# Kernel tuning notes

Hardware: AMD Instinct MI355X
Metric: run time of the kernel (lower is better)

## Reference

```python
import jax, jax.numpy as jnp
import numpy as np

C = 512
C8 = C // 8


def setup_inputs() -> dict:
    key = jax.random.key(0)
    ks = jax.random.split(key, 7)
    B, W = 8, 2048
    x = jax.random.normal(ks[0], (B, C, W), dtype=jnp.float32)
    # 1x1 Conv1d == pointwise linear: weight [out, in], bias [out]
    s_q = 1.0 / np.sqrt(C)
    Wq = jax.random.uniform(ks[1], (C8, C), jnp.float32, -s_q, s_q)
    bq = jax.random.uniform(ks[2], (C8,), jnp.float32, -s_q, s_q)
    Wk = jax.random.uniform(ks[3], (C8, C), jnp.float32, -s_q, s_q)
    bk = jax.random.uniform(ks[4], (C8,), jnp.float32, -s_q, s_q)
    Wv = jax.random.uniform(ks[5], (C, C), jnp.float32, -s_q, s_q)
    bv = jax.random.uniform(ks[6], (C,), jnp.float32, -s_q, s_q)
    gamma = jnp.zeros((1,), dtype=jnp.float32)
    return {"x": x, "Wq": Wq, "bq": bq, "Wk": Wk, "bk": bk, "Wv": Wv, "bv": bv, "gamma": gamma}


def reference(x, Wq, bq, Wk, bk, Wv, bv, gamma):
    # x: [B, C, W]; 1x1 conv projections (pointwise linear over channel dim)
    q = jnp.einsum('oc,bcw->bwo', Wq, x) + bq            # [B, W, C/8]
    k = jnp.einsum('oc,bcw->bow', Wk, x) + bk[:, None]   # [B, C/8, W]
    v = jnp.einsum('oc,bcw->bow', Wv, x) + bv[:, None]   # [B, C, W]
    # attention[b, i, j] over keys j (no scaling, matching the original)
    attn = jax.nn.softmax(jnp.einsum('bwo,bov->bwv', q, k), axis=-1)  # [B, W, W]
    out = jnp.einsum('bcj,bij->bci', v, attn)            # [B, C, W]
    return gamma[0] * out + x
```

## Files before the change

kernel.cpp:

```cpp
#include <hip/hip_runtime.h>
#include <stdint.h>

#define B_  8
#define C_  512
#define CO_ 64
#define W_  2048
#define R_  640
#define LOG2E 1.4426950408889634f

typedef float f32x4 __attribute__((ext_vector_type(4)));
typedef float f32x16 __attribute__((ext_vector_type(16)));
typedef __bf16 bf16x8 __attribute__((ext_vector_type(8)));
typedef __bf16 bf16x2 __attribute__((ext_vector_type(2)));
typedef unsigned u32x2 __attribute__((ext_vector_type(2)));
typedef unsigned u32x4 __attribute__((ext_vector_type(4)));
typedef unsigned short u16;
typedef u16 u16x8 __attribute__((ext_vector_type(8)));
typedef u16 u16x4 __attribute__((ext_vector_type(4)));

static __device__ __forceinline__ float exp2g(float f){
  return __builtin_amdgcn_exp2f(f);
}
static __device__ __forceinline__ u16 f2b(float f){
  union { float f; unsigned u; } v; v.f = f;
  unsigned r = v.u + 0x7FFFu + ((v.u >> 16) & 1u);
  return (u16)(r >> 16);
}
static __device__ __forceinline__ bf16x8 ldb(const u16* p){
  return __builtin_bit_cast(bf16x8, *(const u16x8*)p);
}
static __device__ __forceinline__ f32x4 mfma16(bf16x8 a, bf16x8 b, f32x4 c){
  return __builtin_amdgcn_mfma_f32_16x16x32_bf16(a, b, c, 0, 0, 0);
}
static __device__ __forceinline__ f32x16 mfma32(bf16x8 a, bf16x8 b, f32x16 c){
  return __builtin_amdgcn_mfma_f32_32x32x16_bf16(a, b, c, 0, 0, 0);
}
static __device__ __forceinline__ void pl32swap(unsigned &a, unsigned &b){
  asm("v_permlane32_swap_b32 %0, %1" : "+v"(a), "+v"(b));
}
static __device__ __forceinline__ float red_sum32(float v){
  unsigned a = __builtin_bit_cast(unsigned, v), b = a;
  pl32swap(a, b);
  return __builtin_bit_cast(float, a) + __builtin_bit_cast(float, b);
}
static __device__ __forceinline__ unsigned pkbf(float lo, float hi){
  bf16x2 t; t[0] = (__bf16)lo; t[1] = (__bf16)hi;
  return __builtin_bit_cast(unsigned, t);
}
static __device__ __forceinline__ void barrier_lds_only(){
  asm volatile("s_waitcnt lgkmcnt(0)" ::: "memory");
  __builtin_amdgcn_s_barrier();
}

__global__ __launch_bounds__(256) void prep_w(
    const float* __restrict__ Wq, const float* __restrict__ bq,
    const float* __restrict__ Wk, const float* __restrict__ bk,
    const float* __restrict__ Wv, const float* __restrict__ bv,
    u16* __restrict__ Wall, float* __restrict__ ball){
  int e = blockIdx.x * 256 + threadIdx.x;
  if (e < R_ * C_){
    int r = e >> 9, c = e & (C_ - 1);
    float w;
    if (r < 64)       w = Wq[r * C_ + c] * LOG2E;
    else if (r < 128) w = Wk[(r - 64) * C_ + c];
    else              w = Wv[(r - 128) * C_ + c];
    Wall[e] = f2b(w);
  }
  if (e < R_){
    float bb;
    if (e < 64)       bb = bq[e] * LOG2E;
    else if (e < 128) bb = bk[e - 64];
    else              bb = bv[e - 128];
    ball[e] = bb;
  }
}

__global__ __launch_bounds__(256) void xpose(const float* __restrict__ x,
                                             u16* __restrict__ xbT){
  __shared__ float t[32][33];
  int b = blockIdx.z, c0 = blockIdx.y * 32, w0 = blockIdx.x * 32;
  int tx = threadIdx.x & 31, ty = threadIdx.x >> 5;
  const float* xb = x + (size_t)b * C_ * W_;
  #pragma unroll
  for (int k = 0; k < 4; k++)
    t[ty + k * 8][tx] = xb[(size_t)(c0 + ty + k * 8) * W_ + w0 + tx];
  __syncthreads();
  u16* ob = xbT + (size_t)b * W_ * C_;
  #pragma unroll
  for (int k = 0; k < 4; k++)
    ob[(size_t)(w0 + ty + k * 8) * C_ + c0 + tx] = f2b(t[tx][ty + k * 8]);
}

#define PADW 40
__global__ __launch_bounds__(256) void gemm_proj(
    const u16* __restrict__ Wall, const float* __restrict__ ball,
    const u16* __restrict__ xbT, u16* __restrict__ qf,
    u16* __restrict__ kf, u16* __restrict__ vf){
  __shared__ u16 at[64][PADW];
  __shared__ u16 bt[64][PADW];
  int b = blockIdx.z;
  int m0 = blockIdx.y * 64, n0 = blockIdx.x * 64;
  int tid = threadIdx.x, lane = tid & 63, wid = tid >> 6;
  int wm = wid >> 1, wn = wid & 1;
  int g = lane >> 4, r = lane & 15;
  const u16* xb = xbT + (size_t)b * W_ * C_;
  f32x4 acc[2][2] = {};
  int srow = tid >> 2, sseg = (tid & 3) * 8;
  for (int kk = 0; kk < 16; kk++){
    int c0 = kk * 32;
    *(u16x8*)&at[srow][sseg] = *(const u16x8*)&Wall[(size_t)(m0 + srow) * C_ + c0 + sseg];
    *(u16x8*)&bt[srow][sseg] = *(const u16x8*)&xb[(size_t)(n0 + srow) * C_ + c0 + sseg];
    barrier_lds_only();
    bf16x8 a0 = ldb(&at[wm * 32 +  0 + r][g * 8]);
    bf16x8 a1 = ldb(&at[wm * 32 + 16 + r][g * 8]);
    bf16x8 b0 = ldb(&bt[wn * 32 +  0 + r][g * 8]);
    bf16x8 b1 = ldb(&bt[wn * 32 + 16 + r][g * 8]);
    acc[0][0] = mfma16(a0, b0, acc[0][0]);
    acc[0][1] = mfma16(a0, b1, acc[0][1]);
    acc[1][0] = mfma16(a1, b0, acc[1][0]);
    acc[1][1] = mfma16(a1, b1, acc[1][1]);
    barrier_lds_only();
  }
  #pragma unroll
  for (int i = 0; i < 2; i++){
    #pragma unroll
    for (int n = 0; n < 2; n++){
      int rbase = m0 + wm * 32 + i * 16 + g * 4;
      int wcol  = n0 + wn * 32 + n * 16 + r;
      if (m0 < 128){
        u16* base = (m0 == 0 ? qf : kf) + (size_t)b * W_ * CO_;
        int o0 = (rbase & 63);
        int oc = o0 >> 4, h2 = (o0 >> 3) & 1, e0 = o0 & 7;
        u16x4 pk;
        #pragma unroll
        for (int t = 0; t < 4; t++) pk[t] = f2b(acc[i][n][t] + ball[rbase + t]);
        *(u16x4*)&base[((size_t)((wcol >> 5) * 4 + oc) * 64 + h2 * 32 + (wcol & 31)) * 8 + e0] = pk;
      } else {
        u16* vb = vf + (size_t)b * C_ * W_;
        int jt = wcol >> 4, h2 = (wcol >> 3) & 1, e = wcol & 7;
        #pragma unroll
        for (int t = 0; t < 4; t++){
          int c = rbase + t - 128;
          vb[((size_t)((c >> 5) * (W_ / 16) + jt) * 64 + h2 * 32 + (c & 31)) * 8 + e] =
              f2b(acc[i][n][t] + ball[rbase + t]);
        }
      }
    }
  }
}

__global__ __launch_bounds__(512, 2) void attn14(
    const u16* __restrict__ qf, const u16* __restrict__ kf,
    const u16* __restrict__ vf, const float* __restrict__ x,
    const float* __restrict__ gamma, float* __restrict__ out){
  __shared__ u16 pb[2][2][32][132];
  __shared__ float lredf[2][4][32];
  int tid = threadIdx.x, lane = tid & 63, wv = tid >> 6;
  int jw = wv & 3, iw = wv >> 2;
  int bid = blockIdx.x;
  int b = bid & 7;
  int i0 = (bid >> 3) * 64;
  int cbase = wv * 64;
  int li = lane & 31, hi = lane >> 5;
  int swz = (li & 7) << 3;
  const u16* qfb = qf + (size_t)b * W_ * CO_;
  const u16* kfb = kf + (size_t)b * W_ * CO_;
  const u16* vfb = vf + (size_t)b * C_ * W_;

  bf16x8 fq[4];
  {
    const u16* qp = &qfb[(size_t)((i0 >> 5) + iw) * 4 * 512 + lane * 8];
    #pragma unroll
    for (int oc = 0; oc < 4; oc++) fq[oc] = ldb(qp + oc * 512);
  }

  const u16* kp = &kfb[(size_t)jw * 2048 + lane * 8];
  const u16* vpt0 = &vfb[(size_t)(cbase >> 5) * (W_ / 16) * 512 + lane * 8];
  const u16* vpt1 = vpt0 + (size_t)(W_ / 16) * 512;

  f32x16 acc00 = {}, acc01 = {}, acc10 = {}, acc11 = {};
  f32x4 lacc = {};

  auto sphase = [&](bf16x8 (&fk)[4], int bsel){
    f32x16 S = {};
    S = mfma32(fk[0], fq[0], S);
    S = mfma32(fk[1], fq[1], S);
    S = mfma32(fk[2], fq[2], S);
    S = mfma32(fk[3], fq[3], S);
    float p[16];
    #pragma unroll
    for (int t = 0; t < 16; t++) p[t] = exp2g(S[t]);
    #pragma unroll
    for (int t = 0; t < 4; t++)
      lacc[t] += ((p[t] + p[4 + t]) + (p[8 + t] + p[12 + t]));
    #pragma unroll
    for (int B = 0; B < 4; B++){
      unsigned lo = pkbf(p[4 * B + 0], p[4 * B + 1]);
      unsigned h2 = pkbf(p[4 * B + 2], p[4 * B + 3]);
      int j0 = (jw * 32 + 8 * B + 4 * hi) ^ swz;
      u32x2 wpair = {lo, h2};
      *(u32x2*)&pb[bsel][iw][li][j0] = wpair;
    }
  };
  auto pfrag = [&](int bsel, int it, int jj, int kj) -> bf16x8 {
    int j0 = (jj * 32 + kj * 16 + 8 * hi) ^ swz;
    u16x4 a = *(const u16x4*)&pb[bsel][it][li][j0];
    u16x4 c = *(const u16x4*)&pb[bsel][it][li][j0 + 4];
    u16x8 w = {a[0], a[1], a[2], a[3], c[0], c[1], c[2], c[3]};
    return __builtin_bit_cast(bf16x8, w);
  };
  auto loadV = [&](bf16x8 (&fv)[4], int off){
    fv[0] = ldb(vpt0 + off); fv[1] = ldb(vpt0 + off + 512);
    fv[2] = ldb(vpt1 + off); fv[3] = ldb(vpt1 + off + 512);
  };
  auto PV = [&](bf16x8 (&fv)[4], int bsel, int jj){
    bf16x8 p00 = pfrag(bsel, 0, jj, 0), p01 = pfrag(bsel, 0, jj, 1);
    bf16x8 p10 = pfrag(bsel, 1, jj, 0), p11 = pfrag(bsel, 1, jj, 1);
    __builtin_amdgcn_s_setprio(1);
    acc00 = mfma32(fv[0], p00, acc00); acc00 = mfma32(fv[1], p01, acc00);
    acc10 = mfma32(fv[2], p00, acc10); acc10 = mfma32(fv[3], p01, acc10);
    acc01 = mfma32(fv[0], p10, acc01); acc01 = mfma32(fv[1], p11, acc01);
    acc11 = mfma32(fv[2], p10, acc11); acc11 = mfma32(fv[3], p11, acc11);
    __builtin_amdgcn_s_setprio(0);
  };

  bf16x8 fvX[4], fvY[4];
  {
    bf16x8 fk[4];
    #pragma unroll
    for (int oc = 0; oc < 4; oc++) fk[oc] = ldb(kp + oc * 512);
    sphase(fk, 0);
  }
  loadV(fvX, 0);
  barrier_lds_only();

  int cur = 0;
  for (int m = 0; m < 16; ++m){
    bf16x8 fkN[4];
    if (m < 15){
      const u16* kpn = kp + 8192;
      #pragma unroll
      for (int oc = 0; oc < 4; oc++) fkN[oc] = ldb(kpn + oc * 512);
    }
    loadV(fvY, 1024);
    PV(fvX, cur, 0);
    loadV(fvX, 2048);
    PV(fvY, cur, 1);
    loadV(fvY, 3072);
    PV(fvX, cur, 2);
    if (m < 15) loadV(fvX, 4096);
    PV(fvY, cur, 3);
    if (m < 15) sphase(fkN, cur ^ 1);
    kp += 8192; vpt0 += 4096; vpt1 += 4096;
    barrier_lds_only();
    cur ^= 1;
  }

  float l = (lacc[0] + lacc[1]) + (lacc[2] + lacc[3]);
  l = red_sum32(l);
  if (hi == 0) lredf[iw][jw][li] = l;
  __syncthreads();
  float lf0 = (lredf[0][0][li] + lredf[0][1][li]) + (lredf[0][2][li] + lredf[0][3][li]);
  float lf1 = (lredf[1][0][li] + lredf[1][1][li]) + (lredf[1][2][li] + lredf[1][3][li]);

  float gm = gamma[0];
  float iv0 = 1.f / lf0, iv1 = 1.f / lf1;
  const float* xb = x + (size_t)b * C_ * W_;
  float* ob = out + (size_t)b * C_ * W_;
  auto epi = [&](f32x16 &acc, int ct, int it, float iv){
    int icol = i0 + it * 32 + li;
    #pragma unroll
    for (int t = 0; t < 16; t++){
      int crow = (t & 3) + 8 * (t >> 2) + 4 * hi;
      int c = cbase + ct * 32 + crow;
      ob[(size_t)c * W_ + icol] = gm * (acc[t] * iv) + xb[(size_t)c * W_ + icol];
    }
  };
  epi(acc00, 0, 0, iv0); epi(acc10, 1, 0, iv0);
  epi(acc01, 0, 1, iv1); epi(acc11, 1, 1, iv1);
}

extern "C" void kernel_launch(void* const* d_in, const int* in_sizes, int n_in,
                              void* d_out, int out_size, void* d_ws, size_t ws_size,
                              hipStream_t stream) {
  const float* x     = (const float*)d_in[0];
  const float* Wq    = (const float*)d_in[1];
  const float* bq    = (const float*)d_in[2];
  const float* Wk    = (const float*)d_in[3];
  const float* bk    = (const float*)d_in[4];
  const float* Wv    = (const float*)d_in[5];
  const float* bv    = (const float*)d_in[6];
  const float* gamma = (const float*)d_in[7];
  float* out = (float*)d_out;
  char* ws = (char*)d_ws;
  u16*   Wall = (u16*)  (ws + 0);
  float* ball = (float*)(ws + 655360);
  u16*   xbT  = (u16*)  (ws + 657920);
  u16*   qf   = (u16*)  (ws + 17435136);
  u16*   kf   = (u16*)  (ws + 19532288);
  u16*   vf   = (u16*)  (ws + 21629440);

  prep_w<<<dim3(1280), dim3(256), 0, stream>>>(Wq, bq, Wk, bk, Wv, bv, Wall, ball);
  xpose<<<dim3(64, 16, 8), dim3(256), 0, stream>>>(x, xbT);
  gemm_proj<<<dim3(32, 10, 8), dim3(256), 0, stream>>>(Wall, ball, xbT, qf, kf, vf);
  attn14<<<dim3(256), dim3(512), 0, stream>>>(qf, kf, vf, x, gamma, out);
}
```

Measured before the change: 97.39 us.

## Fuse x transpose into projection GEMM with pre-swizzled weights

```diff
diff --git a/kernel.cpp b/kernel.cpp
--- a/kernel.cpp
+++ b/kernel.cpp
@@ -56,7 +56,7 @@
     const float* __restrict__ Wq, const float* __restrict__ bq,
     const float* __restrict__ Wk, const float* __restrict__ bk,
     const float* __restrict__ Wv, const float* __restrict__ bv,
-    u16* __restrict__ Wall, float* __restrict__ ball){
+    u16* __restrict__ af, float* __restrict__ ball){
   int e = blockIdx.x * 256 + threadIdx.x;
   if (e < R_ * C_){
     int r = e >> 9, c = e & (C_ - 1);
@@ -64,7 +64,9 @@
     if (r < 64)       w = Wq[r * C_ + c] * LOG2E;
     else if (r < 128) w = Wk[(r - 64) * C_ + c];
     else              w = Wv[(r - 128) * C_ + c];
-    Wall[e] = f2b(w);
+    int mt16 = r >> 4, mr = r & 15;
+    int kk = c >> 5, g = (c >> 3) & 3, e8 = c & 7;
+    af[(((size_t)mt16 * 16 + kk) * 64 + g * 16 + mr) * 8 + e8] = f2b(w);
   }
   if (e < R_){
     float bb;
@@ -75,74 +77,92 @@
   }
 }
 
-__global__ __launch_bounds__(256) void xpose(const float* __restrict__ x,
-                                             u16* __restrict__ xbT){
-  __shared__ float t[32][33];
-  int b = blockIdx.z, c0 = blockIdx.y * 32, w0 = blockIdx.x * 32;
-  int tx = threadIdx.x & 31, ty = threadIdx.x >> 5;
+#define PADB 520
+__global__ __launch_bounds__(512) void gemm_fused(
+    const u16* __restrict__ af, const float* __restrict__ ball,
+    const float* __restrict__ x, u16* __restrict__ qf,
+    u16* __restrict__ kf, u16* __restrict__ vf){
+  __shared__ u16 bt[64][PADB];
+  __shared__ float t[32][65];
+  int b = blockIdx.y;
+  int w0 = blockIdx.x * 64;
+  int tid = threadIdx.x, lane = tid & 63, wid = tid >> 6;
+  int ws = wid >> 2, wm = (wid >> 1) & 1, wn = wid & 1;
+  int g = lane >> 4, r = lane & 15;
   const float* xb = x + (size_t)b * C_ * W_;
-  #pragma unroll
-  for (int k = 0; k < 4; k++)
-    t[ty + k * 8][tx] = xb[(size_t)(c0 + ty + k * 8) * W_ + w0 + tx];
-  __syncthreads();
-  u16* ob = xbT + (size_t)b * W_ * C_;
-  #pragma unroll
-  for (int k = 0; k < 4; k++)
-    ob[(size_t)(w0 + ty + k * 8) * C_ + c0 + tx] = f2b(t[tx][ty + k * 8]);
-}
-
-#define PADW 40
-__global__ __launch_bounds__(256) void gemm_proj(
-    const u16* __restrict__ Wall, const float* __restrict__ ball,
-    const u16* __restrict__ xbT, u16* __restrict__ qf,
-    u16* __restrict__ kf, u16* __restrict__ vf){
-  __shared__ u16 at[64][PADW];
-  __shared__ u16 bt[64][PADW];
-  int b = blockIdx.z;
-  int m0 = blockIdx.y * 64, n0 = blockIdx.x * 64;
-  int tid = threadIdx.x, lane = tid & 63, wid = tid >> 6;
-  int wm = wid >> 1, wn = wid & 1;
-  int g = lane >> 4, r = lane & 15;
-  const u16* xb = xbT + (size_t)b * W_ * C_;
-  f32x4 acc[2][2] = {};
-  int srow = tid >> 2, sseg = (tid & 3) * 8;
-  for (int kk = 0; kk < 16; kk++){
-    int c0 = kk * 32;
-    *(u16x8*)&at[srow][sseg] = *(const u16x8*)&Wall[(size_t)(m0 + srow) * C_ + c0 + sseg];
-    *(u16x8*)&bt[srow][sseg] = *(const u16x8*)&xb[(size_t)(n0 + srow) * C_ + c0 + sseg];
-    barrier_lds_only();
-    bf16x8 a0 = ldb(&at[wm * 32 +  0 + r][g * 8]);
-    bf16x8 a1 = ldb(&at[wm * 32 + 16 + r][g * 8]);
-    bf16x8 b0 = ldb(&bt[wn * 32 +  0 + r][g * 8]);
-    bf16x8 b1 = ldb(&bt[wn * 32 + 16 + r][g * 8]);
-    acc[0][0] = mfma16(a0, b0, acc[0][0]);
-    acc[0][1] = mfma16(a0, b1, acc[0][1]);
-    acc[1][0] = mfma16(a1, b0, acc[1][0]);
-    acc[1][1] = mfma16(a1, b1, acc[1][1]);
-    barrier_lds_only();
-  }
-  #pragma unroll
-  for (int i = 0; i < 2; i++){
-    #pragma unroll
-    for (int n = 0; n < 2; n++){
-      int rbase = m0 + wm * 32 + i * 16 + g * 4;
-      int wcol  = n0 + wn * 32 + n * 16 + r;
-      if (m0 < 128){
-        u16* base = (m0 == 0 ? qf : kf) + (size_t)b * W_ * CO_;
-        int o0 = (rbase & 63);
-        int oc = o0 >> 4, h2 = (o0 >> 3) & 1, e0 = o0 & 7;
-        u16x4 pk;
-        #pragma unroll
-        for (int t = 0; t < 4; t++) pk[t] = f2b(acc[i][n][t] + ball[rbase + t]);
-        *(u16x4*)&base[((size_t)((wcol >> 5) * 4 + oc) * 64 + h2 * 32 + (wcol & 31)) * 8 + e0] = pk;
-      } else {
-        u16* vb = vf + (size_t)b * C_ * W_;
-        int jt = wcol >> 4, h2 = (wcol >> 3) & 1, e = wcol & 7;
-        #pragma unroll
-        for (int t = 0; t < 4; t++){
-          int c = rbase + t - 128;
-          vb[((size_t)((c >> 5) * (W_ / 16) + jt) * 64 + h2 * 32 + (c & 31)) * 8 + e] =
-              f2b(acc[i][n][t] + ball[rbase + t]);
+
+  {
+    int rrow = tid >> 4, wseg = (tid & 15) * 4;
+    int tw = tid >> 3, cseg = (tid & 7) * 4;
+    for (int cc = 0; cc < 16; cc++){
+      const float* xp = &xb[(size_t)(cc * 32 + rrow) * W_ + w0 + wseg];
+      float v0 = xp[0], v1 = xp[1], v2 = xp[2], v3 = xp[3];
+      t[rrow][wseg + 0] = v0; t[rrow][wseg + 1] = v1;
+      t[rrow][wseg + 2] = v2; t[rrow][wseg + 3] = v3;
+      barrier_lds_only();
+      u16x4 pk;
+      #pragma unroll
+      for (int k = 0; k < 4; k++) pk[k] = f2b(t[cseg + k][tw]);
+      *(u16x4*)&bt[tw][cc * 32 + cseg] = pk;
+      barrier_lds_only();
+    }
+  }
+
+  for (int mt = ws; mt < 10; mt += 2){
+    f32x4 acc[2][2] = {};
+    int mt0 = mt * 4 + wm * 2;
+    const u16* ap0 = af + ((size_t)(mt0 * 16) * 64 + lane) * 8;
+    const u16* ap1 = af + ((size_t)((mt0 + 1) * 16) * 64 + lane) * 8;
+    bf16x8 aX0 = ldb(ap0), aX1 = ldb(ap1);
+    bf16x8 aY0, aY1;
+    #pragma unroll
+    for (int kk = 0; kk < 16; kk += 2){
+      aY0 = ldb(ap0 + (kk + 1) * 512);
+      aY1 = ldb(ap1 + (kk + 1) * 512);
+      {
+        bf16x8 b0 = ldb(&bt[wn * 32 +  0 + r][kk * 32 + g * 8]);
+        bf16x8 b1 = ldb(&bt[wn * 32 + 16 + r][kk * 32 + g * 8]);
+        acc[0][0] = mfma16(aX0, b0, acc[0][0]);
+        acc[0][1] = mfma16(aX0, b1, acc[0][1]);
+        acc[1][0] = mfma16(aX1, b0, acc[1][0]);
+        acc[1][1] = mfma16(aX1, b1, acc[1][1]);
+      }
+      if (kk + 2 < 16){
+        aX0 = ldb(ap0 + (kk + 2) * 512);
+        aX1 = ldb(ap1 + (kk + 2) * 512);
+      }
+      {
+        bf16x8 b0 = ldb(&bt[wn * 32 +  0 + r][(kk + 1) * 32 + g * 8]);
+        bf16x8 b1 = ldb(&bt[wn * 32 + 16 + r][(kk + 1) * 32 + g * 8]);
+        acc[0][0] = mfma16(aY0, b0, acc[0][0]);
+        acc[0][1] = mfma16(aY0, b1, acc[0][1]);
+        acc[1][0] = mfma16(aY1, b0, acc[1][0]);
+        acc[1][1] = mfma16(aY1, b1, acc[1][1]);
+      }
+    }
+    #pragma unroll
+    for (int i = 0; i < 2; i++){
+      #pragma unroll
+      for (int n = 0; n < 2; n++){
+        int rbase = mt * 64 + wm * 32 + i * 16 + g * 4;
+        int wcol  = w0 + wn * 32 + n * 16 + r;
+        if (mt < 2){
+          u16* base = (mt == 0 ? qf : kf) + (size_t)b * W_ * CO_;
+          int o0 = (rbase & 63);
+          int oc = o0 >> 4, h2 = (o0 >> 3) & 1, e0 = o0 & 7;
+          u16x4 pk;
+          #pragma unroll
+          for (int tt = 0; tt < 4; tt++) pk[tt] = f2b(acc[i][n][tt] + ball[rbase + tt]);
+          *(u16x4*)&base[((size_t)((wcol >> 5) * 4 + oc) * 64 + h2 * 32 + (wcol & 31)) * 8 + e0] = pk;
+        } else {
+          u16* vb = vf + (size_t)b * C_ * W_;
+          int jt = wcol >> 4, h2 = (wcol >> 3) & 1, e = wcol & 7;
+          #pragma unroll
+          for (int tt = 0; tt < 4; tt++){
+            int c = rbase + tt - 128;
+            vb[((size_t)((c >> 5) * (W_ / 16) + jt) * 64 + h2 * 32 + (c & 31)) * 8 + e] =
+                f2b(acc[i][n][tt] + ball[rbase + tt]);
+          }
         }
       }
     }
@@ -293,15 +313,13 @@
   const float* gamma = (const float*)d_in[7];
   float* out = (float*)d_out;
   char* ws = (char*)d_ws;
-  u16*   Wall = (u16*)  (ws + 0);
+  u16*   af   = (u16*)  (ws + 0);
   float* ball = (float*)(ws + 655360);
-  u16*   xbT  = (u16*)  (ws + 657920);
   u16*   qf   = (u16*)  (ws + 17435136);
   u16*   kf   = (u16*)  (ws + 19532288);
   u16*   vf   = (u16*)  (ws + 21629440);
 
-  prep_w<<<dim3(1280), dim3(256), 0, stream>>>(Wq, bq, Wk, bk, Wv, bv, Wall, ball);
-  xpose<<<dim3(64, 16, 8), dim3(256), 0, stream>>>(x, xbT);
-  gemm_proj<<<dim3(32, 10, 8), dim3(256), 0, stream>>>(Wall, ball, xbT, qf, kf, vf);
+  prep_w<<<dim3(1280), dim3(256), 0, stream>>>(Wq, bq, Wk, bk, Wv, bv, af, ball);
+  gemm_fused<<<dim3(32, 8), dim3(512), 0, stream>>>(af, ball, x, qf, kf, vf);
   attn14<<<dim3(256), dim3(512), 0, stream>>>(qf, kf, vf, x, gamma, out);
 }
```

New measurement: 90.13 us. 1.08x faster.
